# Kernel tuning notes

Measured on AMD Instinct MI355X. Metric: run time of the kernel, lower is better.

The kernel has to match this reference:

```python
import jax, jax.numpy as jnp
import numpy as np

DEPTH = 16
HID = 256
INP = 256
K = 2  # arity of the complete binary tree
TOTAL = (1 << (DEPTH + 1)) - 1  # 131071 nodes, level-order indexed


def setup_inputs() -> dict:
    key = jax.random.key(0)
    ks = jax.random.split(key, 14)
    s = 1.0 / np.sqrt(HID)
    inp = {
        "x": jax.random.normal(ks[0], (TOTAL, INP), jnp.float32),
        "Wi": jax.random.normal(ks[1], (HID, INP), jnp.float32) * s,
        "bi": jax.random.normal(ks[2], (HID,), jnp.float32) * s,
        "Wf": jax.random.normal(ks[3], (HID, INP), jnp.float32) * s,
        "bf": jax.random.normal(ks[4], (HID,), jnp.float32) * s,
        "Wo": jax.random.normal(ks[5], (HID, INP), jnp.float32) * s,
        "bo": jax.random.normal(ks[6], (HID,), jnp.float32) * s,
        "Wu": jax.random.normal(ks[7], (HID, INP), jnp.float32) * s,
        "bu": jax.random.normal(ks[8], (HID,), jnp.float32) * s,
        "Ui": jax.random.normal(ks[9], (HID, HID), jnp.float32) * s,
        "Uo": jax.random.normal(ks[10], (HID, HID), jnp.float32) * s,
        "Uu": jax.random.normal(ks[11], (HID, HID), jnp.float32) * s,
        "Wfk": jax.random.normal(ks[12], (K, HID, HID), jnp.float32) * s,
        "depth": DEPTH,
    }
    return inp


def reference(x, Wi, bi, Wf, bf, Wo, bo, Wu, bu, Ui, Uo, Uu, Wfk, depth):
    sig = jax.nn.sigmoid
    H = Ui.shape[0]
    # leaf level: leaf_forward (no recurrent terms)
    start, n = (1 << depth) - 1, 1 << depth
    xs = x[start:start + n]                      # [n, INP]
    i = sig(xs @ Wi.T + bi)
    o = sig(xs @ Wo.T + bo)
    u = jnp.tanh(xs @ Wu.T + bu)
    c = i * u
    h = o * jnp.tanh(c)
    # internal levels, bottom-up
    for d in range(depth - 1, -1, -1):
        start, n = (1 << d) - 1, 1 << d
        xs = x[start:start + n]                  # [n, INP]
        hc = h.reshape(n, K, H)                  # children h (level-order)
        cc = c.reshape(n, K, H)                  # children c
        Hs = hc.sum(axis=1)                      # sum over children, [n, H]
        i = sig(xs @ Wi.T + bi + Hs @ Ui.T)
        o = sig(xs @ Wo.T + bo + Hs @ Uo.T)
        u = jnp.tanh(xs @ Wu.T + bu + Hs @ Uu.T)
        # per-child-position forget gate; original applies wf{k} to the SUM of all children h
        fx = xs @ Wf.T + bf                      # [n, H]
        ukfh = jnp.einsum('ni,koi->nko', Hs, Wfk)  # [n, K, H]
        f = sig(fx[:, None, :] + ukfh)
        c = i * u + (f * cc).sum(axis=1)
        h = o * jnp.tanh(c)
    return jnp.stack([h, c])  # [2, 1, H]: root (h, c)
```

## Files before the change

kernel.cpp:

```cpp
#include <hip/hip_runtime.h>
#include <math.h>


#define LEAF_N 65536

typedef __attribute__((ext_vector_type(8))) short bf16x8;
typedef __attribute__((ext_vector_type(4))) float f32x4;
typedef unsigned short u16;

__device__ __forceinline__ float fast_sig(float x) {
    return __builtin_amdgcn_rcpf(1.0f + __expf(-x));
}
__device__ __forceinline__ float fast_tanh(float x) {
    return 2.0f * __builtin_amdgcn_rcpf(1.0f + __expf(-2.0f * x)) - 1.0f;
}

__device__ __forceinline__ u16 f2bf(float f) {
    union { float f; unsigned u; } v; v.f = f;
    unsigned r = v.u + 0x7fffu + ((v.u >> 16) & 1u);
    return (u16)(r >> 16);
}

__host__ __device__ __forceinline__ size_t zrowOff(int d) {
    return (size_t)(65536 - (2 << d)) * 512;
}

__device__ __forceinline__ void gld_lds16(const u16* g, u16* s) {
    __builtin_amdgcn_global_load_lds(
        (const __attribute__((address_space(1))) void*)g,
        (__attribute__((address_space(3))) void*)s, 16, 0, 0);
}

__global__ __launch_bounds__(256) void pack_weights(
    const float* __restrict__ Wi, const float* __restrict__ bi,
    const float* __restrict__ Wf, const float* __restrict__ bf,
    const float* __restrict__ Wo, const float* __restrict__ bo,
    const float* __restrict__ Wu, const float* __restrict__ bu,
    const float* __restrict__ Ui, const float* __restrict__ Uo,
    const float* __restrict__ Uu, const float* __restrict__ Wfk,
    u16* __restrict__ Wrow, u16* __restrict__ Wfrag, u16* __restrict__ WleafRow,
    float* __restrict__ bbig, float* __restrict__ bleaf)
{
    int idx = blockIdx.x * 256 + threadIdx.x;
    const int NWB = 1280 * 512;
    const int NWL = 768 * 256;

    auto bigval = [&](int row, int k) -> float {
        int g = row >> 8, rr = row & 255;
        if (k < 256) {
            const float* W = (g == 0) ? Wi : (g == 1) ? Wo : (g == 2) ? Wu : Wf;
            return W[rr * 256 + k];
        }
        int kk = k - 256;
        return (g == 0) ? Ui[rr * 256 + kk]
             : (g == 1) ? Uo[rr * 256 + kk]
             : (g == 2) ? Uu[rr * 256 + kk]
             : (g == 3) ? Wfk[rr * 256 + kk]
                        : Wfk[65536 + rr * 256 + kk];
    };

    if (idx < NWB) {
        Wrow[idx] = f2bf(bigval(idx >> 9, idx & 511));
    } else if (idx < 2 * NWB) {
        int q = idx - NWB;
        int j = q & 7, l = (q >> 3) & 63, kc = (q >> 9) & 15, nt = q >> 13;
        int row = nt * 16 + (l & 15);
        int k = kc * 32 + ((l >> 4) << 3) + j;
        Wfrag[q] = f2bf(bigval(row, k));
    } else if (idx < 2 * NWB + NWL) {
        int q = idx - 2 * NWB;
        int r = q >> 8, k = q & 255;
        int g = r >> 8, rr = r & 255;
        const float* W = (g == 0) ? Wi : (g == 1) ? Wo : Wu;
        WleafRow[q] = f2bf(W[rr * 256 + k]);
    } else if (idx < 2 * NWB + NWL + 1280) {
        int r = idx - 2 * NWB - NWL;
        int g = r >> 8, rr = r & 255;
        bbig[r] = (g == 0) ? bi[rr] : (g == 1) ? bo[rr] : (g == 2) ? bu[rr] : bf[rr];
    } else if (idx < 2 * NWB + NWL + 1280 + 768) {
        int r = idx - 2 * NWB - NWL - 1280;
        int g = r >> 8, rr = r & 255;
        bleaf[r] = (g == 0) ? bi[rr] : (g == 1) ? bo[rr] : bu[rr];
    }
}

__global__ __launch_bounds__(256) void cvt_all(
    const float* __restrict__ x, u16* __restrict__ Zrow,
    u16* __restrict__ Ztiles, u16* __restrict__ Xbf)
{
    int idx = blockIdx.x * 256 + threadIdx.x;
    if (idx >= 131071 * 32) return;
    int row = idx >> 5, k8 = idx & 31;
    const float* s = x + (size_t)row * 256 + k8 * 8;
    u16 r[8];
#pragma unroll
    for (int i = 0; i < 8; i++) r[i] = f2bf(s[i]);
    if (row < 65535) {
        int d = 31 - __clz(row + 1);
        int jn = row - ((1 << d) - 1);
        if (d >= 5) {
            *(uint4*)(Zrow + zrowOff(d) + (size_t)jn * 512 + k8 * 8) = *(uint4*)r;
        } else {
            int kc = k8 >> 2;
            int l = (jn & 15) + ((k8 & 3) << 4);
            size_t dst = (size_t)(4 - d) * 8192 + ((size_t)kc * 64 + l) * 8;
            *(uint4*)(Ztiles + dst) = *(uint4*)r;
        }
    } else {
        int jn = row - 65535;
        *(uint4*)(Xbf + (size_t)jn * 256 + k8 * 8) = *(uint4*)r;
    }
}

__global__ __launch_bounds__(256) void gate_gemm(
    const u16* __restrict__ A, int lda, int M,
    const u16* __restrict__ B, int ldb, int Kdim,
    const float* __restrict__ bias, _Float16* __restrict__ G, int NC)
{
    __shared__ u16 As[128 * 64];
    __shared__ u16 Bs[128 * 64];

    const int tid  = threadIdx.x;
    const int wave = tid >> 6;
    const int lane = tid & 63;
    const int bm = blockIdx.x * 128;
    const int bn = blockIdx.y * 128;

    const int wm = (wave >> 1) * 64;
    const int wn = (wave & 1) * 64;
    const int lm = lane & 15;
    const int q4 = lane >> 4;

    const int srow = lane >> 3;
    const int scol = ((lane & 7) ^ srow) * 8;

    f32x4 acc[4][4] = {};

    for (int k0 = 0; k0 < Kdim; k0 += 64) {
#pragma unroll
        for (int q = 0; q < 4; ++q) {
            const int grp = wave * 4 + q;
            const int r = grp * 8 + srow;
            gld_lds16(A + (size_t)(bm + r) * lda + k0 + scol,
                      As + (size_t)grp * 512 + lane * 8);
            gld_lds16(B + (size_t)(bn + r) * ldb + k0 + scol,
                      Bs + (size_t)grp * 512 + lane * 8);
        }
        __syncthreads();

#pragma unroll
        for (int kk = 0; kk < 64; kk += 32) {
            const int sw = (((kk >> 3) + q4) ^ (lm & 7)) << 3;
            bf16x8 af[4], bfr[4];
#pragma unroll
            for (int i = 0; i < 4; i++)
                af[i] = *(const bf16x8*)(As + (wm + i * 16 + lm) * 64 + sw);
#pragma unroll
            for (int j = 0; j < 4; j++)
                bfr[j] = *(const bf16x8*)(Bs + (wn + j * 16 + lm) * 64 + sw);
#pragma unroll
            for (int i = 0; i < 4; i++)
#pragma unroll
                for (int j = 0; j < 4; j++)
                    acc[i][j] = __builtin_amdgcn_mfma_f32_16x16x32_bf16(
                        af[i], bfr[j], acc[i][j], 0, 0, 0);
        }
        __syncthreads();
    }

    const int cr0 = q4 * 4;
    const int ccc = lm;
#pragma unroll
    for (int i = 0; i < 4; i++) {
#pragma unroll
        for (int reg = 0; reg < 4; reg++) {
            int r = bm + wm + i * 16 + cr0 + reg;
            if (r >= M) continue;
#pragma unroll
            for (int j = 0; j < 4; j++) {
                int cn = bn + wn + j * 16 + ccc;
                float v = acc[i][j][reg] + bias[cn];
                float a = ((cn >> 8) == 2) ? fast_tanh(v) : fast_sig(v);
                G[(size_t)r * NC + cn] = (_Float16)a;
            }
        }
    }
}

template<bool LEAF>
__global__ __launch_bounds__(256) void combine(
    const _Float16* __restrict__ G, const float* __restrict__ csrc,
    float* __restrict__ cdst, u16* __restrict__ zrow_parent,
    u16* __restrict__ zfrag_parent)
{
    constexpr int NC = LEAF ? 768 : 1280;
    const int p = blockIdx.x, h = threadIdx.x;
    const _Float16* G0 = G + (size_t)(2 * p) * NC;
    const _Float16* G1 = G0 + NC;
    float i0 = (float)G0[h], o0 = (float)G0[256 + h], u0 = (float)G0[512 + h];
    float i1 = (float)G1[h], o1 = (float)G1[256 + h], u1 = (float)G1[512 + h];
    float c0 = i0 * u0, c1 = i1 * u1;
    if (!LEAF) {
        float f00 = (float)G0[768 + h], f10 = (float)G0[1024 + h];
        float f01 = (float)G1[768 + h], f11 = (float)G1[1024 + h];
        c0 += f00 * csrc[(size_t)(4 * p) * 256 + h]
            + f10 * csrc[(size_t)(4 * p + 1) * 256 + h];
        c1 += f01 * csrc[(size_t)(4 * p + 2) * 256 + h]
            + f11 * csrc[(size_t)(4 * p + 3) * 256 + h];
    }
    float h0 = o0 * fast_tanh(c0), h1 = o1 * fast_tanh(c1);
    cdst[(size_t)(2 * p) * 256 + h] = c0;
    cdst[(size_t)(2 * p) * 256 + 256 + h] = c1;
    u16 hs = f2bf(h0 + h1);
    if (zrow_parent) {
        zrow_parent[(size_t)p * 512 + 256 + h] = hs;
    } else {
        size_t a = (((size_t)8 + (h >> 5)) * 64
                    + (p & 15) + (((h >> 3) & 3) << 4)) * 8 + (h & 7);
        zfrag_parent[a] = hs;
    }
}

__global__ __launch_bounds__(64) void small_gemm(
    const u16* __restrict__ Zpk, const u16* __restrict__ Wfrag,
    const float* __restrict__ bias, float* __restrict__ pre, int n)
{
    const int lane = threadIdx.x;
    const int q = blockIdx.x;
    const int nt0 = (q >> 2) * 16 + (q & 3) * 4;
    const int cc = lane & 15, rq = (lane >> 4) * 4;

    f32x4 acc[4] = {};
    const u16* aB = Zpk + (size_t)lane * 8;
    const u16* bB = Wfrag + ((size_t)nt0 * 16 * 64 + lane) * 8;

    bf16x8 aX, bX[4], aY, bY[4];
    aX = *(const bf16x8*)(aB);
#pragma unroll
    for (int j = 0; j < 4; ++j)
        bX[j] = *(const bf16x8*)(bB + (size_t)(j * 16) * 512);

#pragma unroll
    for (int kc = 0; kc < 16; kc += 2) {
        aY = *(const bf16x8*)(aB + (size_t)(kc + 1) * 512);
#pragma unroll
        for (int j = 0; j < 4; ++j)
            bY[j] = *(const bf16x8*)(bB + (size_t)(j * 16 + kc + 1) * 512);
#pragma unroll
        for (int j = 0; j < 4; ++j)
            acc[j] = __builtin_amdgcn_mfma_f32_16x16x32_bf16(aX, bX[j], acc[j], 0, 0, 0);
        if (kc + 2 < 16) {
            aX = *(const bf16x8*)(aB + (size_t)(kc + 2) * 512);
#pragma unroll
            for (int j = 0; j < 4; ++j)
                bX[j] = *(const bf16x8*)(bB + (size_t)(j * 16 + kc + 2) * 512);
        }
#pragma unroll
        for (int j = 0; j < 4; ++j)
            acc[j] = __builtin_amdgcn_mfma_f32_16x16x32_bf16(aY, bY[j], acc[j], 0, 0, 0);
    }

#pragma unroll
    for (int j = 0; j < 4; ++j) {
        int coln = (nt0 + j) * 16 + cc;
        float bb = bias[coln];
#pragma unroll
        for (int r = 0; r < 4; ++r) {
            int row = rq + r;
            if (row < n) pre[(size_t)row * 1280 + coln] = acc[j][r] + bb;
        }
    }
}

__global__ __launch_bounds__(256) void epi_small(
    const float* __restrict__ pre, const float* __restrict__ csrc,
    float* __restrict__ c_out, u16* __restrict__ zfrag_parent,
    float* __restrict__ root_out, int npairs)
{
    int idx = blockIdx.x * 256 + threadIdx.x;
    if (root_out) {
        int h = idx;
        const float* p = pre;
        float c = fast_sig(p[h]) * fast_tanh(p[512 + h])
                + fast_sig(p[768 + h]) * csrc[h]
                + fast_sig(p[1024 + h]) * csrc[256 + h];
        root_out[h] = fast_sig(p[256 + h]) * fast_tanh(c);
        root_out[256 + h] = c;
        return;
    }
    if (idx >= npairs * 256) return;
    int pI = idx >> 8, h = idx & 255;
    int n0 = 2 * pI;
    const float* p0 = pre + (size_t)n0 * 1280;
    const float* p1 = p0 + 1280;
    float c0 = fast_sig(p0[h]) * fast_tanh(p0[512 + h])
             + fast_sig(p0[768 + h]) * csrc[(size_t)(2 * n0) * 256 + h]
             + fast_sig(p0[1024 + h]) * csrc[(size_t)(2 * n0 + 1) * 256 + h];
    float c1 = fast_sig(p1[h]) * fast_tanh(p1[512 + h])
             + fast_sig(p1[768 + h]) * csrc[(size_t)(2 * n0 + 2) * 256 + h]
             + fast_sig(p1[1024 + h]) * csrc[(size_t)(2 * n0 + 3) * 256 + h];
    float h0 = fast_sig(p0[256 + h]) * fast_tanh(c0);
    float h1 = fast_sig(p1[256 + h]) * fast_tanh(c1);
    c_out[(size_t)n0 * 256 + h] = c0;
    c_out[(size_t)(n0 + 1) * 256 + h] = c1;
    size_t a = (((size_t)8 + (h >> 5)) * 64
                + (pI & 15) + (((h >> 3) & 3) << 4)) * 8 + (h & 7);
    zfrag_parent[a] = f2bf(h0 + h1);
}

extern "C" void kernel_launch(void* const* d_in, const int* in_sizes, int n_in,
                              void* d_out, int out_size, void* d_ws, size_t ws_size,
                              hipStream_t stream)
{
    const float* x   = (const float*)d_in[0];
    const float* Wi  = (const float*)d_in[1];
    const float* bi  = (const float*)d_in[2];
    const float* Wf  = (const float*)d_in[3];
    const float* bf  = (const float*)d_in[4];
    const float* Wo  = (const float*)d_in[5];
    const float* bo  = (const float*)d_in[6];
    const float* Wu  = (const float*)d_in[7];
    const float* bu  = (const float*)d_in[8];
    const float* Ui  = (const float*)d_in[9];
    const float* Uo  = (const float*)d_in[10];
    const float* Uu  = (const float*)d_in[11];
    const float* Wfk = (const float*)d_in[12];
    float* out = (float*)d_out;
    char* ws   = (char*)d_ws;
    (void)ws_size; (void)in_sizes; (void)n_in; (void)out_size;

    size_t off = 0;
    u16* Wrow     = (u16*)(ws + off); off += (size_t)1280 * 512 * 2;
    u16* Wfrag    = (u16*)(ws + off); off += (size_t)1280 * 512 * 2;
    u16* WleafRow = (u16*)(ws + off); off += (size_t)768 * 256 * 2;
    float* bbig   = (float*)(ws + off); off += 1280 * 4;
    float* bleaf  = (float*)(ws + off); off += 768 * 4 + 192;
    u16* Xbf    = (u16*)(ws + off); off += (size_t)65536 * 256 * 2;
    u16* Zrow   = (u16*)(ws + off); off += (size_t)65536 * 512 * 2;
    u16* Ztiles = (u16*)(ws + off); off += (size_t)5 * 8192 * 2;
    float* cA = (float*)(ws + off); off += (size_t)65536 * 256 * 4;
    float* cB = (float*)(ws + off); off += (size_t)32768 * 256 * 4;
    float* pre_small = (float*)(ws + off); off += (size_t)16 * 1280 * 4;
    _Float16* Ghalf = (_Float16*)(ws + off); off += (size_t)65536 * 768 * 2;

    auto ztile = [&](int d) -> u16* { return Ztiles + (size_t)(4 - d) * 8192; };

    pack_weights<<<5897, 256, 0, stream>>>(Wi, bi, Wf, bf, Wo, bo, Wu, bu,
                                           Ui, Uo, Uu, Wfk, Wrow, Wfrag, WleafRow,
                                           bbig, bleaf);
    cvt_all<<<16385, 256, 0, stream>>>(x, Zrow, Ztiles, Xbf);

    gate_gemm<<<dim3(LEAF_N / 128, 6), 256, 0, stream>>>(
        Xbf, 256, LEAF_N, WleafRow, 256, 256, bleaf, Ghalf, 768);
    combine<true><<<LEAF_N / 2, 256, 0, stream>>>(
        Ghalf, nullptr, cA, Zrow + zrowOff(15), nullptr);

    for (int d = 15; d >= 5; d--) {
        int n = 1 << d;
        float* csrc = (d & 1) ? cA : cB;
        float* cdst = (d & 1) ? cB : cA;
        gate_gemm<<<dim3((n + 127) / 128, 10), 256, 0, stream>>>(
            Zrow + zrowOff(d), 512, n, Wrow, 512, 512, bbig, Ghalf, 1280);
        if (d >= 6)
            combine<false><<<n / 2, 256, 0, stream>>>(
                Ghalf, csrc, cdst, Zrow + zrowOff(d - 1), nullptr);
        else
            combine<false><<<n / 2, 256, 0, stream>>>(
                Ghalf, csrc, cdst, nullptr, ztile(4));
    }

    for (int d = 4; d >= 1; d--) {
        int n = 1 << d;
        float* csrc = (d & 1) ? cA : cB;
        float* cdst = (d & 1) ? cB : cA;
        small_gemm<<<20, 64, 0, stream>>>(ztile(d), Wfrag, bbig, pre_small, n);
        epi_small<<<n / 2, 256, 0, stream>>>(pre_small, csrc, cdst,
                                             ztile(d - 1), nullptr, n / 2);
    }

    small_gemm<<<20, 64, 0, stream>>>(ztile(0), Wfrag, bbig, pre_small, 1);
    epi_small<<<1, 256, 0, stream>>>(pre_small, cB, nullptr, nullptr, out, 0);
}
```

Baseline: 825.0 us.

## Keep full-K A tile resident in LDS and stream fragment-packed weights from global

Rewrites the gate GEMM so each 512-thread block loads its whole 128-row A slab (all K) into LDS once, then loops over 256-column output chunks, reading B directly from a pre-packed MFMA fragment layout in global memory instead of staging it through LDS. The first chunk overlaps the A load with compute using staged vmcnt waits and barriers. Small levels split the column chunks across grid.y to keep enough blocks in flight. This removes repeated A reloads and the per-K-step syncs, but relies on weights staying hot in L2/cache and uses up to 128KB of dynamic LDS per block, which limits occupancy.

```diff
diff --git a/kernel.cpp b/kernel.cpp
--- a/kernel.cpp
+++ b/kernel.cpp
@@ -29,6 +29,10 @@
     __builtin_amdgcn_global_load_lds(
         (const __attribute__((address_space(1))) void*)g,
         (__attribute__((address_space(3))) void*)s, 16, 0, 0);
+}
+
+template<int N> __device__ __forceinline__ void wait_vm() {
+    asm volatile("s_waitcnt vmcnt(%0)" :: "n"(N) : "memory");
 }
 
 __global__ __launch_bounds__(256) void pack_weights(
@@ -38,7 +42,7 @@
     const float* __restrict__ Wu, const float* __restrict__ bu,
     const float* __restrict__ Ui, const float* __restrict__ Uo,
     const float* __restrict__ Uu, const float* __restrict__ Wfk,
-    u16* __restrict__ Wrow, u16* __restrict__ Wfrag, u16* __restrict__ WleafRow,
+    u16* __restrict__ Wfrag, u16* __restrict__ WleafFrag,
     float* __restrict__ bbig, float* __restrict__ bleaf)
 {
     int idx = blockIdx.x * 256 + threadIdx.x;
@@ -60,25 +64,25 @@
     };
 
     if (idx < NWB) {
-        Wrow[idx] = f2bf(bigval(idx >> 9, idx & 511));
-    } else if (idx < 2 * NWB) {
-        int q = idx - NWB;
+        int q = idx;
         int j = q & 7, l = (q >> 3) & 63, kc = (q >> 9) & 15, nt = q >> 13;
         int row = nt * 16 + (l & 15);
         int k = kc * 32 + ((l >> 4) << 3) + j;
         Wfrag[q] = f2bf(bigval(row, k));
-    } else if (idx < 2 * NWB + NWL) {
-        int q = idx - 2 * NWB;
-        int r = q >> 8, k = q & 255;
-        int g = r >> 8, rr = r & 255;
+    } else if (idx < NWB + NWL) {
+        int q = idx - NWB;
+        int j = q & 7, l = (q >> 3) & 63, kc = (q >> 9) & 7, nt = q >> 12;
+        int row = nt * 16 + (l & 15);
+        int k = kc * 32 + ((l >> 4) << 3) + j;
+        int g = row >> 8, rr = row & 255;
         const float* W = (g == 0) ? Wi : (g == 1) ? Wo : Wu;
-        WleafRow[q] = f2bf(W[rr * 256 + k]);
-    } else if (idx < 2 * NWB + NWL + 1280) {
-        int r = idx - 2 * NWB - NWL;
+        WleafFrag[q] = f2bf(W[rr * 256 + k]);
+    } else if (idx < NWB + NWL + 1280) {
+        int r = idx - NWB - NWL;
         int g = r >> 8, rr = r & 255;
         bbig[r] = (g == 0) ? bi[rr] : (g == 1) ? bo[rr] : (g == 2) ? bu[rr] : bf[rr];
-    } else if (idx < 2 * NWB + NWL + 1280 + 768) {
-        int r = idx - 2 * NWB - NWL - 1280;
+    } else if (idx < NWB + NWL + 1280 + 768) {
+        int r = idx - NWB - NWL - 1280;
         int g = r >> 8, rr = r & 255;
         bleaf[r] = (g == 0) ? bi[rr] : (g == 1) ? bo[rr] : bu[rr];
     }
@@ -112,76 +116,95 @@
     }
 }
 
-__global__ __launch_bounds__(256) void gate_gemm(
-    const u16* __restrict__ A, int lda, int M,
-    const u16* __restrict__ B, int ldb, int Kdim,
-    const float* __restrict__ bias, _Float16* __restrict__ G, int NC)
-{
-    __shared__ u16 As[128 * 64];
-    __shared__ u16 Bs[128 * 64];
+template<int KD, int NCH>
+__global__ __launch_bounds__(512, 2) void gate_gemm(
+    const u16* __restrict__ A, int M,
+    const u16* __restrict__ Wf, const float* __restrict__ bias,
+    _Float16* __restrict__ G, int chunks_per)
+{
+    constexpr int NSL = KD / 64;
+    constexpr int KC  = KD / 32;
+    constexpr int NC  = NCH * 256;
+    extern __shared__ u16 As[];
 
     const int tid  = threadIdx.x;
     const int wave = tid >> 6;
     const int lane = tid & 63;
     const int bm = blockIdx.x * 128;
-    const int bn = blockIdx.y * 128;
-
-    const int wm = (wave >> 1) * 64;
-    const int wn = (wave & 1) * 64;
-    const int lm = lane & 15;
-    const int q4 = lane >> 4;
-
-    const int srow = lane >> 3;
-    const int scol = ((lane & 7) ^ srow) * 8;
-
-    f32x4 acc[4][4] = {};
-
-    for (int k0 = 0; k0 < Kdim; k0 += 64) {
-#pragma unroll
-        for (int q = 0; q < 4; ++q) {
-            const int grp = wave * 4 + q;
-            const int r = grp * 8 + srow;
-            gld_lds16(A + (size_t)(bm + r) * lda + k0 + scol,
-                      As + (size_t)grp * 512 + lane * 8);
-            gld_lds16(B + (size_t)(bn + r) * ldb + k0 + scol,
-                      Bs + (size_t)grp * 512 + lane * 8);
-        }
-        __syncthreads();
-
-#pragma unroll
-        for (int kk = 0; kk < 64; kk += 32) {
-            const int sw = (((kk >> 3) + q4) ^ (lm & 7)) << 3;
-            bf16x8 af[4], bfr[4];
-#pragma unroll
-            for (int i = 0; i < 4; i++)
-                af[i] = *(const bf16x8*)(As + (wm + i * 16 + lm) * 64 + sw);
-#pragma unroll
-            for (int j = 0; j < 4; j++)
-                bfr[j] = *(const bf16x8*)(Bs + (wn + j * 16 + lm) * 64 + sw);
-#pragma unroll
-            for (int i = 0; i < 4; i++)
+    const int nc0 = blockIdx.y * chunks_per;
+    if (nc0 >= NCH) return;
+    int ncEnd = nc0 + chunks_per; if (ncEnd > NCH) ncEnd = NCH;
+
+    {
+        const int srow = lane >> 3;
+        const int scol = ((lane & 7) ^ srow) * 8;
+#pragma unroll
+        for (int kc = 0; kc < NSL; ++kc) {
+#pragma unroll
+            for (int q = 0; q < 2; ++q) {
+                const int g = wave * 2 + q;
+                gld_lds16(A + (size_t)(bm + g * 8 + srow) * KD + kc * 64 + scol,
+                          As + kc * 8192 + g * 512 + lane * 8);
+            }
+        }
+    }
+
+    const int wr = wave >> 2;
+    const int wc = wave & 3;
+    const int wm = wr * 64;
+    const int lm = lane & 15, q4 = lane >> 4;
+
+    const u16* sa = As + (wm + lm) * 64;
+
+    for (int nc = nc0; nc < ncEnd; ++nc) {
+        f32x4 acc[4][4] = {};
+        const u16* wfb = Wf + ((size_t)(nc * 16 + wc * 4) * KC) * 512 + lane * 8;
+
+#pragma unroll
+        for (int kc8 = 0; kc8 < NSL; ++kc8) {
+            if (nc == nc0) {
+#define WVM(k) case k: wait_vm<(2*(NSL-1-(k)) > 0 ? 2*(NSL-1-(k)) : 0)>(); break;
+                switch (kc8) { WVM(0) WVM(1) WVM(2) WVM(3) WVM(4) WVM(5) WVM(6) WVM(7) }
+#undef WVM
+                __builtin_amdgcn_s_barrier();
+                __builtin_amdgcn_sched_barrier(0);
+            }
+#pragma unroll
+            for (int kk = 0; kk < 64; kk += 32) {
+                const int sw = ((((kk >> 3) + q4) ^ (lm & 7)) << 3);
+                const int kc = kc8 * 2 + (kk >> 5);
+                bf16x8 af[4], bfr[4];
+#pragma unroll
+                for (int i = 0; i < 4; i++)
+                    af[i] = *(const bf16x8*)(sa + kc8 * 8192 + i * 1024 + sw);
 #pragma unroll
                 for (int j = 0; j < 4; j++)
-                    acc[i][j] = __builtin_amdgcn_mfma_f32_16x16x32_bf16(
-                        af[i], bfr[j], acc[i][j], 0, 0, 0);
-        }
-        __syncthreads();
-    }
-
-    const int cr0 = q4 * 4;
-    const int ccc = lm;
-#pragma unroll
-    for (int i = 0; i < 4; i++) {
-#pragma unroll
-        for (int reg = 0; reg < 4; reg++) {
-            int r = bm + wm + i * 16 + cr0 + reg;
-            if (r >= M) continue;
+                    bfr[j] = *(const bf16x8*)(wfb + (size_t)(j * KC + kc) * 512);
+#pragma unroll
+                for (int i = 0; i < 4; i++)
+#pragma unroll
+                    for (int j = 0; j < 4; j++)
+                        acc[i][j] = __builtin_amdgcn_mfma_f32_16x16x32_bf16(
+                            af[i], bfr[j], acc[i][j], 0, 0, 0);
+            }
+        }
+
+        const int cr0 = q4 * 4;
+#pragma unroll
+        for (int i = 0; i < 4; i++) {
 #pragma unroll
             for (int j = 0; j < 4; j++) {
-                int cn = bn + wn + j * 16 + ccc;
-                float v = acc[i][j][reg] + bias[cn];
-                float a = ((cn >> 8) == 2) ? fast_tanh(v) : fast_sig(v);
-                G[(size_t)r * NC + cn] = (_Float16)a;
+                const int cg = nc * 256 + wc * 64 + j * 16 + lm;
+                const float bb = bias[cg];
+                const bool istan = ((cg >> 8) == 2);
+#pragma unroll
+                for (int reg = 0; reg < 4; reg++) {
+                    const int rr = bm + wm + i * 16 + cr0 + reg;
+                    if (rr >= M) continue;
+                    float v = acc[i][j][reg] + bb;
+                    G[(size_t)rr * NC + cg] =
+                        (_Float16)(istan ? fast_tanh(v) : fast_sig(v));
+                }
             }
         }
     }
@@ -330,9 +353,8 @@
     (void)ws_size; (void)in_sizes; (void)n_in; (void)out_size;
 
     size_t off = 0;
-    u16* Wrow     = (u16*)(ws + off); off += (size_t)1280 * 512 * 2;
-    u16* Wfrag    = (u16*)(ws + off); off += (size_t)1280 * 512 * 2;
-    u16* WleafRow = (u16*)(ws + off); off += (size_t)768 * 256 * 2;
+    u16* Wfrag     = (u16*)(ws + off); off += (size_t)1280 * 512 * 2;
+    u16* WleafFrag = (u16*)(ws + off); off += (size_t)768 * 256 * 2;
     float* bbig   = (float*)(ws + off); off += 1280 * 4;
     float* bleaf  = (float*)(ws + off); off += 768 * 4 + 192;
     u16* Xbf    = (u16*)(ws + off); off += (size_t)65536 * 256 * 2;
@@ -345,13 +367,22 @@
 
     auto ztile = [&](int d) -> u16* { return Ztiles + (size_t)(4 - d) * 8192; };
 
-    pack_weights<<<5897, 256, 0, stream>>>(Wi, bi, Wf, bf, Wo, bo, Wu, bu,
-                                           Ui, Uo, Uu, Wfk, Wrow, Wfrag, WleafRow,
+    static bool attr_set = false;
+    if (!attr_set) {
+        hipFuncSetAttribute((const void*)gate_gemm<512, 5>,
+                            hipFuncAttributeMaxDynamicSharedMemorySize, 131072);
+        hipFuncSetAttribute((const void*)gate_gemm<256, 3>,
+                            hipFuncAttributeMaxDynamicSharedMemorySize, 65536);
+        attr_set = true;
+    }
+
+    pack_weights<<<3336, 256, 0, stream>>>(Wi, bi, Wf, bf, Wo, bo, Wu, bu,
+                                           Ui, Uo, Uu, Wfk, Wfrag, WleafFrag,
                                            bbig, bleaf);
     cvt_all<<<16385, 256, 0, stream>>>(x, Zrow, Ztiles, Xbf);
 
-    gate_gemm<<<dim3(LEAF_N / 128, 6), 256, 0, stream>>>(
-        Xbf, 256, LEAF_N, WleafRow, 256, 256, bleaf, Ghalf, 768);
+    gate_gemm<256, 3><<<dim3(LEAF_N / 128, 1), 512, 65536, stream>>>(
+        Xbf, LEAF_N, WleafFrag, bleaf, Ghalf, 3);
     combine<true><<<LEAF_N / 2, 256, 0, stream>>>(
         Ghalf, nullptr, cA, Zrow + zrowOff(15), nullptr);
 
@@ -359,8 +390,11 @@
         int n = 1 << d;
         float* csrc = (d & 1) ? cA : cB;
         float* cdst = (d & 1) ? cB : cA;
-        gate_gemm<<<dim3((n + 127) / 128, 10), 256, 0, stream>>>(
-            Zrow + zrowOff(d), 512, n, Wrow, 512, 512, bbig, Ghalf, 1280);
+        int bx = (n + 127) / 128;
+        int cs = 256 / bx; if (cs < 1) cs = 1; if (cs > 5) cs = 5;
+        int cp = (5 + cs - 1) / cs;
+        gate_gemm<512, 5><<<dim3(bx, cs), 512, 131072, stream>>>(
+            Zrow + zrowOff(d), n, Wfrag, bbig, Ghalf, cp);
         if (d >= 6)
             combine<false><<<n / 2, 256, 0, stream>>>(
                 Ghalf, csrc, cdst, Zrow + zrowOff(d - 1), nullptr);
```

Result: slower. 844.2 us (+2.3%).

## Add 256x256-tile double-buffered gate GEMM for leaf and large levels

Applied to the files above, without the earlier changes.

Introduces a templated gate GEMM kernel using 256x256 output tiles, 512 threads, 128KB dynamic LDS with direct global-to-LDS loads, XOR swizzle and double buffering. It is used for the leaf GEMM and tree levels 13-15, while smaller levels keep the old 128x128 kernel. The larger tiles are meant to raise arithmetic intensity and overlap loads with MFMA work on the biggest GEMMs. The costs are heavier register pressure from 32 accumulators per lane, fewer blocks per CU, and a reliance on the row count being a multiple of 256.

```diff
diff --git a/kernel.cpp b/kernel.cpp
--- a/kernel.cpp
+++ b/kernel.cpp
@@ -112,6 +112,89 @@
     }
 }
 
+template<int KD, int NC>
+__global__ __launch_bounds__(512, 2) void gate_gemm_big(
+    const u16* __restrict__ A, const u16* __restrict__ B,
+    const float* __restrict__ bias, _Float16* __restrict__ G)
+{
+    constexpr int NT = KD / 64;
+    extern __shared__ u16 S[];
+
+    const int tid  = threadIdx.x;
+    const int wave = tid >> 6;
+    const int lane = tid & 63;
+    const int bm = blockIdx.x * 256;
+    const int bn = blockIdx.y * 256;
+
+    const int srow = lane >> 3;
+    const int scol = ((lane & 7) ^ srow) * 8;
+
+    const int wr = wave >> 2;
+    const int wc = wave & 3;
+    const int lm = lane & 15, q4 = lane >> 4;
+
+    auto stage = [&](int bi, int t) {
+#pragma unroll
+        for (int q = 0; q < 4; ++q) {
+            const int g = wave * 4 + q;
+            const int r = g * 8 + srow;
+            gld_lds16(A + (size_t)(bm + r) * KD + t * 64 + scol,
+                      S + bi * 32768 + g * 512 + lane * 8);
+            gld_lds16(B + (size_t)(bn + r) * KD + t * 64 + scol,
+                      S + bi * 32768 + 16384 + g * 512 + lane * 8);
+        }
+    };
+
+    f32x4 acc[8][4] = {};
+
+    stage(0, 0);
+    __syncthreads();
+
+#pragma unroll
+    for (int t = 0; t < NT; ++t) {
+        if (t + 1 < NT) stage((t + 1) & 1, t + 1);
+
+        const u16* Ab = S + (t & 1) * 32768;
+        const u16* Bb = Ab + 16384;
+#pragma unroll
+        for (int kk = 0; kk < 64; kk += 32) {
+            const int sw = ((((kk >> 3) + q4) ^ (lm & 7)) << 3);
+            bf16x8 af[8], bfr[4];
+#pragma unroll
+            for (int i = 0; i < 8; i++)
+                af[i] = *(const bf16x8*)(Ab + (wr * 128 + i * 16 + lm) * 64 + sw);
+#pragma unroll
+            for (int j = 0; j < 4; j++)
+                bfr[j] = *(const bf16x8*)(Bb + (wc * 64 + j * 16 + lm) * 64 + sw);
+#pragma unroll
+            for (int i = 0; i < 8; i++)
+#pragma unroll
+                for (int j = 0; j < 4; j++)
+                    acc[i][j] = __builtin_amdgcn_mfma_f32_16x16x32_bf16(
+                        af[i], bfr[j], acc[i][j], 0, 0, 0);
+        }
+        __syncthreads();
+    }
+
+    const int cr0 = q4 * 4;
+#pragma unroll
+    for (int i = 0; i < 8; i++) {
+#pragma unroll
+        for (int j = 0; j < 4; j++) {
+            const int cg = bn + wc * 64 + j * 16 + lm;
+            const float bb = bias[cg];
+            const bool istan = ((cg >> 8) == 2);
+#pragma unroll
+            for (int reg = 0; reg < 4; reg++) {
+                const int rr = bm + wr * 128 + i * 16 + cr0 + reg;
+                float v = acc[i][j][reg] + bb;
+                G[(size_t)rr * NC + cg] =
+                    (_Float16)(istan ? fast_tanh(v) : fast_sig(v));
+            }
+        }
+    }
+}
+
 __global__ __launch_bounds__(256) void gate_gemm(
     const u16* __restrict__ A, int lda, int M,
     const u16* __restrict__ B, int ldb, int Kdim,
@@ -345,13 +428,22 @@
 
     auto ztile = [&](int d) -> u16* { return Ztiles + (size_t)(4 - d) * 8192; };
 
+    static bool attr_set = false;
+    if (!attr_set) {
+        hipFuncSetAttribute((const void*)gate_gemm_big<512, 1280>,
+                            hipFuncAttributeMaxDynamicSharedMemorySize, 131072);
+        hipFuncSetAttribute((const void*)gate_gemm_big<256, 768>,
+                            hipFuncAttributeMaxDynamicSharedMemorySize, 131072);
+        attr_set = true;
+    }
+
     pack_weights<<<5897, 256, 0, stream>>>(Wi, bi, Wf, bf, Wo, bo, Wu, bu,
                                            Ui, Uo, Uu, Wfk, Wrow, Wfrag, WleafRow,
                                            bbig, bleaf);
     cvt_all<<<16385, 256, 0, stream>>>(x, Zrow, Ztiles, Xbf);
 
-    gate_gemm<<<dim3(LEAF_N / 128, 6), 256, 0, stream>>>(
-        Xbf, 256, LEAF_N, WleafRow, 256, 256, bleaf, Ghalf, 768);
+    gate_gemm_big<256, 768><<<dim3(LEAF_N / 256, 3), 512, 131072, stream>>>(
+        Xbf, WleafRow, bleaf, Ghalf);
     combine<true><<<LEAF_N / 2, 256, 0, stream>>>(
         Ghalf, nullptr, cA, Zrow + zrowOff(15), nullptr);
 
@@ -359,8 +451,13 @@
         int n = 1 << d;
         float* csrc = (d & 1) ? cA : cB;
         float* cdst = (d & 1) ? cB : cA;
-        gate_gemm<<<dim3((n + 127) / 128, 10), 256, 0, stream>>>(
-            Zrow + zrowOff(d), 512, n, Wrow, 512, 512, bbig, Ghalf, 1280);
+        if (d >= 13) {
+            gate_gemm_big<512, 1280><<<dim3(n / 256, 5), 512, 131072, stream>>>(
+                Zrow + zrowOff(d), Wrow, bbig, Ghalf);
+        } else {
+            gate_gemm<<<dim3((n + 127) / 128, 10), 256, 0, stream>>>(
+                Zrow + zrowOff(d), 512, n, Wrow, 512, 512, bbig, Ghalf, 1280);
+        }
         if (d >= 6)
             combine<false><<<n / 2, 256, 0, stream>>>(
                 Ghalf, csrc, cdst, Zrow + zrowOff(d - 1), nullptr);
```

New measurement: 774.2 us. 1.07x faster.

## Fuse small tree levels into one persistent LDS kernel and vectorize combine

Applied to the files above, without the earlier changes.

Replaces the per-level small_gemm/epi_small launches for the top five tree levels with a single one-block kernel that keeps c state, preactivations and z tiles in shared memory. This removes about ten tiny launches and their global round trips. Also vectorizes the combine kernel to process eight hidden elements per thread with 16-byte loads and stores. The single block serializes the small GEMMs on one CU and needs a large dynamic LDS allocation.

```diff
diff --git a/kernel.cpp b/kernel.cpp
--- a/kernel.cpp
+++ b/kernel.cpp
@@ -6,6 +6,8 @@
 
 typedef __attribute__((ext_vector_type(8))) short bf16x8;
 typedef __attribute__((ext_vector_type(4))) float f32x4;
+typedef __attribute__((ext_vector_type(8))) float f32x8;
+typedef __attribute__((ext_vector_type(8))) _Float16 f16x8;
 typedef unsigned short u16;
 
 __device__ __forceinline__ float fast_sig(float x) {
@@ -188,124 +190,165 @@
 }
 
 template<bool LEAF>
-__global__ __launch_bounds__(256) void combine(
+__global__ __launch_bounds__(256) void combine_v(
     const _Float16* __restrict__ G, const float* __restrict__ csrc,
     float* __restrict__ cdst, u16* __restrict__ zrow_parent,
     u16* __restrict__ zfrag_parent)
 {
     constexpr int NC = LEAF ? 768 : 1280;
-    const int p = blockIdx.x, h = threadIdx.x;
-    const _Float16* G0 = G + (size_t)(2 * p) * NC;
+    const int t  = threadIdx.x;
+    const int p  = blockIdx.x * 8 + (t >> 5);
+    const int h0 = (t & 31) * 8;
+
+    const _Float16* G0 = G + (size_t)(2 * p) * NC + h0;
     const _Float16* G1 = G0 + NC;
-    float i0 = (float)G0[h], o0 = (float)G0[256 + h], u0 = (float)G0[512 + h];
-    float i1 = (float)G1[h], o1 = (float)G1[256 + h], u1 = (float)G1[512 + h];
-    float c0 = i0 * u0, c1 = i1 * u1;
+
+    f16x8 i0 = *(const f16x8*)(G0);
+    f16x8 o0 = *(const f16x8*)(G0 + 256);
+    f16x8 u0 = *(const f16x8*)(G0 + 512);
+    f16x8 i1 = *(const f16x8*)(G1);
+    f16x8 o1 = *(const f16x8*)(G1 + 256);
+    f16x8 u1 = *(const f16x8*)(G1 + 512);
+
+    f32x8 c0, c1;
+#pragma unroll
+    for (int e = 0; e < 8; e++) {
+        c0[e] = (float)i0[e] * (float)u0[e];
+        c1[e] = (float)i1[e] * (float)u1[e];
+    }
     if (!LEAF) {
-        float f00 = (float)G0[768 + h], f10 = (float)G0[1024 + h];
-        float f01 = (float)G1[768 + h], f11 = (float)G1[1024 + h];
-        c0 += f00 * csrc[(size_t)(4 * p) * 256 + h]
-            + f10 * csrc[(size_t)(4 * p + 1) * 256 + h];
-        c1 += f01 * csrc[(size_t)(4 * p + 2) * 256 + h]
-            + f11 * csrc[(size_t)(4 * p + 3) * 256 + h];
-    }
-    float h0 = o0 * fast_tanh(c0), h1 = o1 * fast_tanh(c1);
-    cdst[(size_t)(2 * p) * 256 + h] = c0;
-    cdst[(size_t)(2 * p) * 256 + 256 + h] = c1;
-    u16 hs = f2bf(h0 + h1);
+        f16x8 f00 = *(const f16x8*)(G0 + 768);
+        f16x8 f10 = *(const f16x8*)(G0 + 1024);
+        f16x8 f01 = *(const f16x8*)(G1 + 768);
+        f16x8 f11 = *(const f16x8*)(G1 + 1024);
+        const float* cs = csrc + (size_t)(4 * p) * 256 + h0;
+        f32x8 cc0 = *(const f32x8*)(cs);
+        f32x8 cc1 = *(const f32x8*)(cs + 256);
+        f32x8 cc2 = *(const f32x8*)(cs + 512);
+        f32x8 cc3 = *(const f32x8*)(cs + 768);
+#pragma unroll
+        for (int e = 0; e < 8; e++) {
+            c0[e] += (float)f00[e] * cc0[e] + (float)f10[e] * cc1[e];
+            c1[e] += (float)f01[e] * cc2[e] + (float)f11[e] * cc3[e];
+        }
+    }
+
+    u16 hs[8];
+#pragma unroll
+    for (int e = 0; e < 8; e++) {
+        float h0v = (float)o0[e] * fast_tanh(c0[e]);
+        float h1v = (float)o1[e] * fast_tanh(c1[e]);
+        hs[e] = f2bf(h0v + h1v);
+    }
+
+    float* cd = cdst + (size_t)(2 * p) * 256 + h0;
+    *(f32x8*)(cd) = c0;
+    *(f32x8*)(cd + 256) = c1;
+
     if (zrow_parent) {
-        zrow_parent[(size_t)p * 512 + 256 + h] = hs;
+        *(uint4*)(zrow_parent + (size_t)p * 512 + 256 + h0) = *(uint4*)hs;
     } else {
-        size_t a = (((size_t)8 + (h >> 5)) * 64
-                    + (p & 15) + (((h >> 3) & 3) << 4)) * 8 + (h & 7);
-        zfrag_parent[a] = hs;
-    }
-}
-
-__global__ __launch_bounds__(64) void small_gemm(
-    const u16* __restrict__ Zpk, const u16* __restrict__ Wfrag,
-    const float* __restrict__ bias, float* __restrict__ pre, int n)
-{
-    const int lane = threadIdx.x;
-    const int q = blockIdx.x;
-    const int nt0 = (q >> 2) * 16 + (q & 3) * 4;
+        size_t a = (((size_t)8 + (h0 >> 5)) * 64
+                    + (p & 15) + (((h0 >> 3) & 3) << 4)) * 8;
+        *(uint4*)(zfrag_parent + a) = *(uint4*)hs;
+    }
+}
+
+__global__ __launch_bounds__(256) void tail_all(
+    const u16* __restrict__ Ztiles, const u16* __restrict__ Wfrag,
+    const float* __restrict__ bbig, const float* __restrict__ c32,
+    float* __restrict__ out)
+{
+    extern __shared__ char L[];
+    float* pre   = (float*)L;
+    float* cbufA = (float*)(L + 81920);
+    float* cbufB = (float*)(L + 81920 + 32768);
+    u16*   zl    = (u16*)(L + 81920 + 49152);
+
+    const int t = threadIdx.x;
+    const int lane = t & 63;
+    const int w = t >> 6;
     const int cc = lane & 15, rq = (lane >> 4) * 4;
 
-    f32x4 acc[4] = {};
-    const u16* aB = Zpk + (size_t)lane * 8;
-    const u16* bB = Wfrag + ((size_t)nt0 * 16 * 64 + lane) * 8;
-
-    bf16x8 aX, bX[4], aY, bY[4];
-    aX = *(const bf16x8*)(aB);
-#pragma unroll
-    for (int j = 0; j < 4; ++j)
-        bX[j] = *(const bf16x8*)(bB + (size_t)(j * 16) * 512);
-
-#pragma unroll
-    for (int kc = 0; kc < 16; kc += 2) {
-        aY = *(const bf16x8*)(aB + (size_t)(kc + 1) * 512);
-#pragma unroll
-        for (int j = 0; j < 4; ++j)
-            bY[j] = *(const bf16x8*)(bB + (size_t)(j * 16 + kc + 1) * 512);
-#pragma unroll
-        for (int j = 0; j < 4; ++j)
-            acc[j] = __builtin_amdgcn_mfma_f32_16x16x32_bf16(aX, bX[j], acc[j], 0, 0, 0);
-        if (kc + 2 < 16) {
-            aX = *(const bf16x8*)(aB + (size_t)(kc + 2) * 512);
-#pragma unroll
-            for (int j = 0; j < 4; ++j)
-                bX[j] = *(const bf16x8*)(bB + (size_t)(j * 16 + kc + 2) * 512);
-        }
-#pragma unroll
-        for (int j = 0; j < 4; ++j)
-            acc[j] = __builtin_amdgcn_mfma_f32_16x16x32_bf16(aY, bY[j], acc[j], 0, 0, 0);
-    }
-
-#pragma unroll
-    for (int j = 0; j < 4; ++j) {
-        int coln = (nt0 + j) * 16 + cc;
-        float bb = bias[coln];
-#pragma unroll
-        for (int r = 0; r < 4; ++r) {
-            int row = rq + r;
-            if (row < n) pre[(size_t)row * 1280 + coln] = acc[j][r] + bb;
-        }
-    }
-}
-
-__global__ __launch_bounds__(256) void epi_small(
-    const float* __restrict__ pre, const float* __restrict__ csrc,
-    float* __restrict__ c_out, u16* __restrict__ zfrag_parent,
-    float* __restrict__ root_out, int npairs)
-{
-    int idx = blockIdx.x * 256 + threadIdx.x;
-    if (root_out) {
-        int h = idx;
-        const float* p = pre;
-        float c = fast_sig(p[h]) * fast_tanh(p[512 + h])
-                + fast_sig(p[768 + h]) * csrc[h]
-                + fast_sig(p[1024 + h]) * csrc[256 + h];
-        root_out[h] = fast_sig(p[256 + h]) * fast_tanh(c);
-        root_out[256 + h] = c;
-        return;
-    }
-    if (idx >= npairs * 256) return;
-    int pI = idx >> 8, h = idx & 255;
-    int n0 = 2 * pI;
-    const float* p0 = pre + (size_t)n0 * 1280;
-    const float* p1 = p0 + 1280;
-    float c0 = fast_sig(p0[h]) * fast_tanh(p0[512 + h])
-             + fast_sig(p0[768 + h]) * csrc[(size_t)(2 * n0) * 256 + h]
-             + fast_sig(p0[1024 + h]) * csrc[(size_t)(2 * n0 + 1) * 256 + h];
-    float c1 = fast_sig(p1[h]) * fast_tanh(p1[512 + h])
-             + fast_sig(p1[768 + h]) * csrc[(size_t)(2 * n0 + 2) * 256 + h]
-             + fast_sig(p1[1024 + h]) * csrc[(size_t)(2 * n0 + 3) * 256 + h];
-    float h0 = fast_sig(p0[256 + h]) * fast_tanh(c0);
-    float h1 = fast_sig(p1[256 + h]) * fast_tanh(c1);
-    c_out[(size_t)n0 * 256 + h] = c0;
-    c_out[(size_t)(n0 + 1) * 256 + h] = c1;
-    size_t a = (((size_t)8 + (h >> 5)) * 64
-                + (pI & 15) + (((h >> 3) & 3) << 4)) * 8 + (h & 7);
-    zfrag_parent[a] = f2bf(h0 + h1);
+    for (int i = t; i < 32 * 256; i += 256) cbufA[i] = c32[i];
+    __syncthreads();
+
+    float* csrc = cbufA;
+    float* cdst = cbufB;
+
+    for (int d = 4; d >= 0; --d) {
+        const int n = 1 << d;
+
+        if (d < 4) {
+            const u16* xs = Ztiles + (size_t)(4 - d) * 8192;
+            for (int i = t * 8; i < 4096; i += 256 * 8)
+                *(uint4*)(zl + i) = *(const uint4*)(xs + i);
+            __syncthreads();
+        }
+        const u16* Z = (d == 4) ? Ztiles : (const u16*)zl;
+
+        for (int it = 0; it < 5; ++it) {
+            const int q = it * 4 + w;
+            const int nt0 = (q >> 2) * 16 + (q & 3) * 4;
+            f32x4 acc[4] = {};
+            const u16* aB = Z + (size_t)lane * 8;
+            const u16* bB = Wfrag + ((size_t)nt0 * 16 * 64 + lane) * 8;
+#pragma unroll
+            for (int kc = 0; kc < 16; ++kc) {
+                bf16x8 aX = *(const bf16x8*)(aB + (size_t)kc * 512);
+#pragma unroll
+                for (int j = 0; j < 4; ++j) {
+                    bf16x8 bX = *(const bf16x8*)(bB + (size_t)(j * 16 + kc) * 512);
+                    acc[j] = __builtin_amdgcn_mfma_f32_16x16x32_bf16(
+                        aX, bX, acc[j], 0, 0, 0);
+                }
+            }
+#pragma unroll
+            for (int j = 0; j < 4; ++j) {
+                int coln = (nt0 + j) * 16 + cc;
+                float bb = bbig[coln];
+#pragma unroll
+                for (int r = 0; r < 4; ++r) {
+                    int row = rq + r;
+                    if (row < n) pre[row * 1280 + coln] = acc[j][r] + bb;
+                }
+            }
+        }
+        __syncthreads();
+
+        if (d > 0) {
+            const int npairs = n / 2;
+            const int h = t;
+            for (int pI = 0; pI < npairs; ++pI) {
+                const float* p0 = pre + (size_t)(2 * pI) * 1280;
+                const float* p1 = p0 + 1280;
+                float c0 = fast_sig(p0[h]) * fast_tanh(p0[512 + h])
+                         + fast_sig(p0[768 + h]) * csrc[(4 * pI) * 256 + h]
+                         + fast_sig(p0[1024 + h]) * csrc[(4 * pI + 1) * 256 + h];
+                float c1 = fast_sig(p1[h]) * fast_tanh(p1[512 + h])
+                         + fast_sig(p1[768 + h]) * csrc[(4 * pI + 2) * 256 + h]
+                         + fast_sig(p1[1024 + h]) * csrc[(4 * pI + 3) * 256 + h];
+                float h0v = fast_sig(p0[256 + h]) * fast_tanh(c0);
+                float h1v = fast_sig(p1[256 + h]) * fast_tanh(c1);
+                cdst[(2 * pI) * 256 + h] = c0;
+                cdst[(2 * pI + 1) * 256 + h] = c1;
+                size_t a = (((size_t)8 + (h >> 5)) * 64
+                            + pI + (((h >> 3) & 3) << 4)) * 8 + (h & 7);
+                zl[a] = f2bf(h0v + h1v);
+            }
+        } else {
+            const int h = t;
+            const float* p = pre;
+            float c = fast_sig(p[h]) * fast_tanh(p[512 + h])
+                    + fast_sig(p[768 + h]) * csrc[h]
+                    + fast_sig(p[1024 + h]) * csrc[256 + h];
+            out[h] = fast_sig(p[256 + h]) * fast_tanh(c);
+            out[256 + h] = c;
+        }
+        __syncthreads();
+
+        float* tmp = csrc; csrc = cdst; cdst = tmp;
+    }
 }
 
 extern "C" void kernel_launch(void* const* d_in, const int* in_sizes, int n_in,
@@ -340,10 +383,14 @@
     u16* Ztiles = (u16*)(ws + off); off += (size_t)5 * 8192 * 2;
     float* cA = (float*)(ws + off); off += (size_t)65536 * 256 * 4;
     float* cB = (float*)(ws + off); off += (size_t)32768 * 256 * 4;
-    float* pre_small = (float*)(ws + off); off += (size_t)16 * 1280 * 4;
     _Float16* Ghalf = (_Float16*)(ws + off); off += (size_t)65536 * 768 * 2;
 
-    auto ztile = [&](int d) -> u16* { return Ztiles + (size_t)(4 - d) * 8192; };
+    static bool attr_set = false;
+    if (!attr_set) {
+        hipFuncSetAttribute((const void*)tail_all,
+                            hipFuncAttributeMaxDynamicSharedMemorySize, 147456);
+        attr_set = true;
+    }
 
     pack_weights<<<5897, 256, 0, stream>>>(Wi, bi, Wf, bf, Wo, bo, Wu, bu,
                                            Ui, Uo, Uu, Wfk, Wrow, Wfrag, WleafRow,
@@ -352,7 +399,7 @@
 
     gate_gemm<<<dim3(LEAF_N / 128, 6), 256, 0, stream>>>(
         Xbf, 256, LEAF_N, WleafRow, 256, 256, bleaf, Ghalf, 768);
-    combine<true><<<LEAF_N / 2, 256, 0, stream>>>(
+    combine_v<true><<<LEAF_N / 16, 256, 0, stream>>>(
         Ghalf, nullptr, cA, Zrow + zrowOff(15), nullptr);
 
     for (int d = 15; d >= 5; d--) {
@@ -362,22 +409,12 @@
         gate_gemm<<<dim3((n + 127) / 128, 10), 256, 0, stream>>>(
             Zrow + zrowOff(d), 512, n, Wrow, 512, 512, bbig, Ghalf, 1280);
         if (d >= 6)
-            combine<false><<<n / 2, 256, 0, stream>>>(
+            combine_v<false><<<n / 16, 256, 0, stream>>>(
                 Ghalf, csrc, cdst, Zrow + zrowOff(d - 1), nullptr);
         else
-            combine<false><<<n / 2, 256, 0, stream>>>(
-                Ghalf, csrc, cdst, nullptr, ztile(4));
-    }
-
-    for (int d = 4; d >= 1; d--) {
-        int n = 1 << d;
-        float* csrc = (d & 1) ? cA : cB;
-        float* cdst = (d & 1) ? cB : cA;
-        small_gemm<<<20, 64, 0, stream>>>(ztile(d), Wfrag, bbig, pre_small, n);
-        epi_small<<<n / 2, 256, 0, stream>>>(pre_small, csrc, cdst,
-                                             ztile(d - 1), nullptr, n / 2);
-    }
-
-    small_gemm<<<20, 64, 0, stream>>>(ztile(0), Wfrag, bbig, pre_small, 1);
-    epi_small<<<1, 256, 0, stream>>>(pre_small, cB, nullptr, nullptr, out, 0);
-}
+            combine_v<false><<<n / 16, 256, 0, stream>>>(
+                Ghalf, csrc, cdst, nullptr, Ztiles);
+    }
+
+    tail_all<<<1, 256, 147456, stream>>>(Ztiles, Wfrag, bbig, cB, out);
+}
```

After: 942.8 us. 14.3% more time.
